# Optimization experiments

Hardware: AMD Instinct MI355X
Metric: run time of the kernel (lower is better)

## Reference

```python
import jax, jax.numpy as jnp
import numpy as np
from jax import lax

B, T, C, F = 32, 128, 64, 64
K, KH, KW = 128, 3, 64  # filters, kernel height (over channels axis), kernel width (= F -> F'=1)
BN_EPS = 1e-3  # keras BatchNormalization default epsilon


def setup_inputs() -> dict:
    key = jax.random.key(0)
    k1, k2 = jax.random.split(key)
    return {
        "x": jax.random.normal(k1, (B, T, C, F), dtype=jnp.float32),
        "conv_w": jax.random.normal(k2, (KH, KW, 1, K), dtype=jnp.float32) * 0.05,
        "conv_b": jnp.zeros((K,), dtype=jnp.float32),
        "bn_gamma": jnp.ones((T,), dtype=jnp.float32),
        "bn_beta": jnp.zeros((T,), dtype=jnp.float32),
        "bn_mean": jnp.zeros((T,), dtype=jnp.float32),
        "bn_var": jnp.ones((T,), dtype=jnp.float32),
    }


def reference(x, conv_w, conv_b, bn_gamma, bn_beta, bn_mean, bn_var):
    # Original loops Conv2D over each time step; we fold T into batch -> one conv.
    b, t, c, f = x.shape
    xr = x.reshape(b * t, c, f, 1)  # NHWC, spatial = (channels, features), 1 in-channel
    y = lax.conv_general_dilated(
        xr, conv_w, window_strides=(1, 1), padding="VALID",
        dimension_numbers=("NHWC", "HWIO", "NHWC"))
    y = y + conv_b  # (B*T, C'=c-KH+1, F'=1, K)
    cp = y.shape[1]
    y = y.reshape(b, t, cp, K)  # F'==1 squeezed; equals concat(axis=-1)+transposes in original
    # Dropout is identity at inference. BatchNorm (inference) over last axis of the
    # concatenated tensor (B, C', K, T) -> params indexed by T here.
    scale = (bn_gamma / jnp.sqrt(bn_var + BN_EPS))[None, :, None, None]
    shift = (bn_beta - bn_mean * bn_gamma / jnp.sqrt(bn_var + BN_EPS))[None, :, None, None]
    y = y * scale + shift
    y = jax.nn.relu(y)
    return y  # (B, T, C', K) -- matches original final transpose [0,3,1,2]
```

## Files before the change

### kernel.cpp

```cpp
#include <hip/hip_runtime.h>
#include <hip/hip_bf16.h>

#define NB   32
#define NT   128
#define NC   64
#define NF   64
#define NK   128
#define NKH  3
#define NCP  62
#define NJ   192
#define BN_EPS 1e-3f

#define XCHUNKS      576
#define WROW_CHUNKS  25
#define WCHUNKS      (NK * WROW_CHUNKS)

typedef __attribute__((ext_vector_type(8))) short short8;
typedef __attribute__((ext_vector_type(4))) float floatx4;

__device__ __forceinline__ short f2bf(float f) {
    __hip_bfloat16 h = __float2bfloat16(f);
    return *reinterpret_cast<short*>(&h);
}

__device__ __forceinline__ int swz(int c) { return c ^ ((c >> 3) & 7); }

__global__ __launch_bounds__(256) void conv_w_to_bf16T(
    const float* __restrict__ w, short* __restrict__ wT)
{
    int idx = blockIdx.x * 256 + threadIdx.x;
    int n = idx / NJ;
    int j = idx - n * NJ;
    wT[idx] = f2bf(w[(size_t)j * NK + n]);
}

__global__ __launch_bounds__(256) void tccnn_mfma(
    const float* __restrict__ x, const short* __restrict__ wT,
    const float* __restrict__ bias, const float* __restrict__ gamma,
    const float* __restrict__ beta, const float* __restrict__ mean,
    const float* __restrict__ var, float* __restrict__ out)
{
    __shared__ short xsh[XCHUNKS * 8];
    __shared__ short wsh[WCHUNKS * 8];

    const int bt  = blockIdx.x;
    const int tid = threadIdx.x;
    const int t   = bt & (NT - 1);

    short8* xs8 = (short8*)xsh;
    short8* ws8 = (short8*)wsh;

    const float4* xbase = (const float4*)(x + (size_t)bt * (NC * NF));
    #pragma unroll
    for (int i = 0; i < 2; ++i) {
        int c = tid + i * 256;
        float4 v0 = xbase[2 * c];
        float4 v1 = xbase[2 * c + 1];
        short8 p;
        p[0] = f2bf(v0.x); p[1] = f2bf(v0.y); p[2] = f2bf(v0.z); p[3] = f2bf(v0.w);
        p[4] = f2bf(v1.x); p[5] = f2bf(v1.y); p[6] = f2bf(v1.z); p[7] = f2bf(v1.w);
        xs8[swz(c)] = p;
    }
    if (tid < 64) {
        short8 z = {0,0,0,0,0,0,0,0};
        xs8[swz(512 + tid)] = z;
    }

    const short8* wTg = (const short8*)wT;
    #pragma unroll
    for (int i = 0; i < 12; ++i) {
        int g = tid + i * 256;
        int n = g / 24;
        int r = g - n * 24;
        ws8[n * WROW_CHUNKS + r] = wTg[g];
    }
    __syncthreads();

    const int wv   = tid >> 6;
    const int lane = tid & 63;
    const int col  = lane & 15;
    const int q    = lane >> 4;

    const int mbase = wv * 16;
    const int arow  = mbase + col;

    floatx4 acc[8];
    #pragma unroll
    for (int nt = 0; nt < 8; ++nt) acc[nt] = (floatx4){0.f, 0.f, 0.f, 0.f};

    #pragma unroll
    for (int s = 0; s < 6; ++s) {
        short8 a = xs8[swz(8 * arow + 4 * s + q)];
        short8 b[8];
        #pragma unroll
        for (int nt = 0; nt < 8; ++nt)
            b[nt] = ws8[(nt * 16 + col) * WROW_CHUNKS + 4 * s + q];
        #pragma unroll
        for (int nt = 0; nt < 8; ++nt)
            acc[nt] = __builtin_amdgcn_mfma_f32_16x16x32_bf16(a, b[nt], acc[nt], 0, 0, 0);
    }

    const float scale = gamma[t] * rsqrtf(var[t] + BN_EPS);
    const float shift = beta[t] - mean[t] * scale;

    float* obase = out + (size_t)bt * (NCP * NK);
    #pragma unroll
    for (int nt = 0; nt < 8; ++nt) {
        const int k  = nt * 16 + col;
        const float bv = bias[k];
        #pragma unroll
        for (int reg = 0; reg < 4; ++reg) {
            const int cp = mbase + q * 4 + reg;
            if (cp < NCP) {
                float v = (acc[nt][reg] + bv) * scale + shift;
                obase[(size_t)cp * NK + k] = v > 0.f ? v : 0.f;
            }
        }
    }
}

extern "C" void kernel_launch(void* const* d_in, const int* in_sizes, int n_in,
                              void* d_out, int out_size, void* d_ws, size_t ws_size,
                              hipStream_t stream) {
    const float* x     = (const float*)d_in[0];
    const float* w     = (const float*)d_in[1];
    const float* bias  = (const float*)d_in[2];
    const float* gamma = (const float*)d_in[3];
    const float* beta  = (const float*)d_in[4];
    const float* mean  = (const float*)d_in[5];
    const float* var   = (const float*)d_in[6];
    float* out = (float*)d_out;
    short* wT  = (short*)d_ws;

    conv_w_to_bf16T<<<dim3(96), dim3(256), 0, stream>>>(w, wT);
    tccnn_mfma<<<dim3(NB * NT), dim3(256), 0, stream>>>(
        x, wT, bias, gamma, beta, mean, var, out);
}
```

Baseline: 216.1 us.

## Load MFMA fragments directly from global memory, dropping shared-memory staging

Precomputes the weight operand in the exact per-lane MFMA fragment layout so each wave reads B fragments straight from global (L2-cached) memory. The x tile is also loaded directly into registers as A fragments, reading overlapping rows from global memory with a clamp at the tail of the buffer. This removes all LDS use and the block barrier, which should raise occupancy. The cost is redundant global and L2 traffic for the weights in every block.

```diff
diff --git a/kernel.cpp b/kernel.cpp
--- a/kernel.cpp
+++ b/kernel.cpp
@@ -6,14 +6,8 @@
 #define NC   64
 #define NF   64
 #define NK   128
-#define NKH  3
 #define NCP  62
-#define NJ   192
 #define BN_EPS 1e-3f
-
-#define XCHUNKS      576
-#define WROW_CHUNKS  25
-#define WCHUNKS      (NK * WROW_CHUNKS)
 
 typedef __attribute__((ext_vector_type(8))) short short8;
 typedef __attribute__((ext_vector_type(4))) float floatx4;
@@ -23,81 +17,66 @@
     return *reinterpret_cast<short*>(&h);
 }
 
-__device__ __forceinline__ int swz(int c) { return c ^ ((c >> 3) & 7); }
-
-__global__ __launch_bounds__(256) void conv_w_to_bf16T(
-    const float* __restrict__ w, short* __restrict__ wT)
+__global__ __launch_bounds__(256) void build_bfrag(
+    const float* __restrict__ w, short8* __restrict__ bfrag)
 {
-    int idx = blockIdx.x * 256 + threadIdx.x;
-    int n = idx / NJ;
-    int j = idx - n * NJ;
-    wT[idx] = f2bf(w[(size_t)j * NK + n]);
+    int idx  = blockIdx.x * 256 + threadIdx.x;
+    int lane = idx & 63;
+    int ts   = idx >> 6;
+    int nt   = ts / 6;
+    int s    = ts - nt * 6;
+    int col  = lane & 15, q = lane >> 4;
+    int n    = nt * 16 + col;
+    int j0   = s * 32 + q * 8;
+    short8 p;
+    #pragma unroll
+    for (int e = 0; e < 8; ++e) p[e] = f2bf(w[(size_t)(j0 + e) * NK + n]);
+    bfrag[idx] = p;
 }
 
-__global__ __launch_bounds__(256) void tccnn_mfma(
-    const float* __restrict__ x, const short* __restrict__ wT,
+__global__ __launch_bounds__(256, 4) void tccnn_mfma2(
+    const float* __restrict__ x, const short8* __restrict__ bfrag,
     const float* __restrict__ bias, const float* __restrict__ gamma,
     const float* __restrict__ beta, const float* __restrict__ mean,
     const float* __restrict__ var, float* __restrict__ out)
 {
-    __shared__ short xsh[XCHUNKS * 8];
-    __shared__ short wsh[WCHUNKS * 8];
-
-    const int bt  = blockIdx.x;
-    const int tid = threadIdx.x;
-    const int t   = bt & (NT - 1);
-
-    short8* xs8 = (short8*)xsh;
-    short8* ws8 = (short8*)wsh;
-
-    const float4* xbase = (const float4*)(x + (size_t)bt * (NC * NF));
-    #pragma unroll
-    for (int i = 0; i < 2; ++i) {
-        int c = tid + i * 256;
-        float4 v0 = xbase[2 * c];
-        float4 v1 = xbase[2 * c + 1];
-        short8 p;
-        p[0] = f2bf(v0.x); p[1] = f2bf(v0.y); p[2] = f2bf(v0.z); p[3] = f2bf(v0.w);
-        p[4] = f2bf(v1.x); p[5] = f2bf(v1.y); p[6] = f2bf(v1.z); p[7] = f2bf(v1.w);
-        xs8[swz(c)] = p;
-    }
-    if (tid < 64) {
-        short8 z = {0,0,0,0,0,0,0,0};
-        xs8[swz(512 + tid)] = z;
-    }
-
-    const short8* wTg = (const short8*)wT;
-    #pragma unroll
-    for (int i = 0; i < 12; ++i) {
-        int g = tid + i * 256;
-        int n = g / 24;
-        int r = g - n * 24;
-        ws8[n * WROW_CHUNKS + r] = wTg[g];
-    }
-    __syncthreads();
-
+    const int bt   = blockIdx.x;
+    const int tid  = threadIdx.x;
     const int wv   = tid >> 6;
     const int lane = tid & 63;
     const int col  = lane & 15;
     const int q    = lane >> 4;
+    const int t    = bt & (NT - 1);
+    const int row  = wv * 16 + col;
 
-    const int mbase = wv * 16;
-    const int arow  = mbase + col;
+    const float4* xg = (const float4*)x;
+    const long maxi  = (long)NB * NT * 1024 - 2;
+    long base4 = (long)bt * 1024 + row * 16 + q * 2;
+    short8 afrag[6];
+    #pragma unroll
+    for (int s = 0; s < 6; ++s) {
+        long i0 = base4 + s * 8;
+        i0 = i0 > maxi ? maxi : i0;
+        float4 v0 = xg[i0];
+        float4 v1 = xg[i0 + 1];
+        short8 p;
+        p[0] = f2bf(v0.x); p[1] = f2bf(v0.y); p[2] = f2bf(v0.z); p[3] = f2bf(v0.w);
+        p[4] = f2bf(v1.x); p[5] = f2bf(v1.y); p[6] = f2bf(v1.z); p[7] = f2bf(v1.w);
+        afrag[s] = p;
+    }
 
     floatx4 acc[8];
     #pragma unroll
     for (int nt = 0; nt < 8; ++nt) acc[nt] = (floatx4){0.f, 0.f, 0.f, 0.f};
 
     #pragma unroll
-    for (int s = 0; s < 6; ++s) {
-        short8 a = xs8[swz(8 * arow + 4 * s + q)];
-        short8 b[8];
+    for (int nt = 0; nt < 8; ++nt) {
+        short8 b[6];
         #pragma unroll
-        for (int nt = 0; nt < 8; ++nt)
-            b[nt] = ws8[(nt * 16 + col) * WROW_CHUNKS + 4 * s + q];
+        for (int s = 0; s < 6; ++s) b[s] = bfrag[(nt * 6 + s) * 64 + lane];
         #pragma unroll
-        for (int nt = 0; nt < 8; ++nt)
-            acc[nt] = __builtin_amdgcn_mfma_f32_16x16x32_bf16(a, b[nt], acc[nt], 0, 0, 0);
+        for (int s = 0; s < 6; ++s)
+            acc[nt] = __builtin_amdgcn_mfma_f32_16x16x32_bf16(afrag[s], b[s], acc[nt], 0, 0, 0);
     }
 
     const float scale = gamma[t] * rsqrtf(var[t] + BN_EPS);
@@ -110,7 +89,7 @@
         const float bv = bias[k];
         #pragma unroll
         for (int reg = 0; reg < 4; ++reg) {
-            const int cp = mbase + q * 4 + reg;
+            const int cp = wv * 16 + q * 4 + reg;
             if (cp < NCP) {
                 float v = (acc[nt][reg] + bv) * scale + shift;
                 obase[(size_t)cp * NK + k] = v > 0.f ? v : 0.f;
@@ -130,9 +109,9 @@
     const float* mean  = (const float*)d_in[5];
     const float* var   = (const float*)d_in[6];
     float* out = (float*)d_out;
-    short* wT  = (short*)d_ws;
+    short8* bfrag = (short8*)d_ws;
 
-    conv_w_to_bf16T<<<dim3(96), dim3(256), 0, stream>>>(w, wT);
-    tccnn_mfma<<<dim3(NB * NT), dim3(256), 0, stream>>>(
-        x, wT, bias, gamma, beta, mean, var, out);
+    build_bfrag<<<dim3(12), dim3(256), 0, stream>>>(w, bfrag);
+    tccnn_mfma2<<<dim3(NB * NT), dim3(256), 0, stream>>>(
+        x, bfrag, bias, gamma, beta, mean, var, out);
 }
```

Result: slower. 226.0 us (+4.6%).
